# Kernel optimization log

Measured on AMD Instinct MI355X. Metric: run time of the kernel, lower is better.

Reference implementation:

```python
import jax, jax.numpy as jnp
import numpy as np

B, S, HID = 2, 1024, 2048
H, D, KV = 32, 64, 8          # query heads, head dim, kv heads (GQA)
INNER = H * D                 # 2048
KV_DIM = KV * D               # 512


def setup_inputs() -> dict:
    key = jax.random.key(0)
    ks = jax.random.split(key, 12)
    s = 0.02
    return {
        "query": jax.random.normal(ks[0], (B, S, HID), jnp.float32),
        "key": jax.random.normal(ks[1], (B, S, HID), jnp.float32),
        "value": jax.random.normal(ks[2], (B, S, HID), jnp.float32),
        "mask": jnp.zeros((B, 1, S, S), jnp.float32),
        "position_bias": jax.random.normal(ks[3], (1, H, S, S), jnp.float32),
        "Wq": jax.random.normal(ks[4], (HID, INNER), jnp.float32) * s,
        "bq": jnp.zeros((INNER,), jnp.float32),
        "Wk": jax.random.normal(ks[5], (HID, KV_DIM), jnp.float32) * s,
        "bk": jnp.zeros((KV_DIM,), jnp.float32),
        "Wv": jax.random.normal(ks[6], (HID, KV_DIM), jnp.float32) * s,
        "bv": jnp.zeros((KV_DIM,), jnp.float32),
        "Wo": jax.random.normal(ks[7], (INNER, HID), jnp.float32) * s,
        "bo": jnp.zeros((HID,), jnp.float32),
    }


def reference(query, key, value, mask, position_bias, Wq, bq, Wk, bk, Wv, bv, Wo, bo):
    # projections (torch nn.Linear equivalent, weights stored [in,out])
    q = (query @ Wq + bq).reshape(B, S, H, D)     # [B,S,H,D]
    k = (key @ Wk + bk).reshape(B, S, KV, D)      # [B,S,KV,D]
    v = (value @ Wv + bv).reshape(B, S, KV, D)
    rep = H // KV
    k = jnp.repeat(k, rep, axis=2)                # GQA repeat_kv -> [B,S,H,D]
    v = jnp.repeat(v, rep, axis=2)
    scores = jnp.einsum("bqhd,bkhd->bhqk", q, k)  # [B,H,S,S]
    scores = (scores + position_bias) * (1.0 / jnp.sqrt(jnp.float32(D)))
    scores = scores + mask
    probs = jax.nn.softmax(scores.astype(jnp.float32), axis=-1).astype(q.dtype)
    out = jnp.einsum("bhqk,bkhd->bqhd", probs, v).reshape(B, S, INNER)
    return out @ Wo + bo                          # [B,S,HID]
```

## Files before the change

kernel.cpp:

```cpp
#include <hip/hip_runtime.h>
#include <stdint.h>


#define DEVI __device__ __forceinline__

typedef __attribute__((ext_vector_type(8))) short bf16x8;
typedef __attribute__((ext_vector_type(4))) float f32x4;
typedef __attribute__((ext_vector_type(4))) float flt4;
typedef __attribute__((ext_vector_type(8))) unsigned short u16x8;
typedef __attribute__((ext_vector_type(4))) unsigned short u16x4;

DEVI unsigned short f2bf(float f){
  union{float f;uint32_t u;}v; v.f=f;
  uint32_t u=v.u;
  u += 0x7FFFu + ((u>>16)&1u);
  return (unsigned short)(u>>16);
}

DEVI uint32_t cvt_pk_bf16(float lo, float hi){
  uint32_t r;
  asm("v_cvt_pk_bf16_f32 %0, %1, %2" : "=v"(r) : "v"(lo), "v"(hi));
  return r;
}

DEVI float fexp2(float x){
#if __has_builtin(__builtin_amdgcn_exp2f)
  return __builtin_amdgcn_exp2f(x);
#else
  return exp2f(x);
#endif
}

DEVI void gload16(const void* g, void* l){
  __builtin_amdgcn_global_load_lds((const __attribute__((address_space(1))) void*)g,
                                   (__attribute__((address_space(3))) void*)l, 16, 0, 0);
}

__global__ void prep_k(const float* __restrict__ q, const float* __restrict__ k,
                       const float* __restrict__ v,
                       unsigned short* __restrict__ qb, unsigned short* __restrict__ kb,
                       unsigned short* __restrict__ vb,
                       const float* __restrict__ Wq, const float* __restrict__ Wk,
                       const float* __restrict__ Wv, const float* __restrict__ Wo,
                       unsigned short* __restrict__ WqT, unsigned short* __restrict__ WkT,
                       unsigned short* __restrict__ WvT, unsigned short* __restrict__ WoT){
  __shared__ float tile[64][65];
  int bid = blockIdx.x;
  if (bid < 6144){
    int z = bid>>11;
    int i = (bid&2047)*256 + threadIdx.x;
    const float* src = z==0 ? q : (z==1 ? k : v);
    unsigned short* dst = z==0 ? qb : (z==1 ? kb : vb);
    const flt4* s = (const flt4*)src;
    flt4 a = s[2*i], b = s[2*i+1];
    u16x8 o;
    o[0]=f2bf(a.x); o[1]=f2bf(a.y); o[2]=f2bf(a.z); o[3]=f2bf(a.w);
    o[4]=f2bf(b.x); o[5]=f2bf(b.y); o[6]=f2bf(b.z); o[7]=f2bf(b.w);
    ((u16x8*)dst)[i] = o;
    return;
  }
  int id = bid - 6144;
  const int K = 2048;
  const float* W; unsigned short* WT; int N, tt;
  if (id < 1024)      { W=Wq; WT=WqT; N=2048; tt=id; }
  else if (id < 1280) { W=Wk; WT=WkT; N=512;  tt=id-1024; }
  else if (id < 1536) { W=Wv; WT=WvT; N=512;  tt=id-1280; }
  else                { W=Wo; WT=WoT; N=2048; tt=id-1536; }
  int sh = (N==2048) ? 5 : 3;
  int n0 = (tt & ((1<<sh)-1))*64, k0 = (tt >> sh)*64;
  int t = threadIdx.x;
  int r = t>>4, c4 = (t&15)*4;
  #pragma unroll
  for (int i=0;i<4;i++){
    flt4 vv = *(const flt4*)&W[(size_t)(k0 + r + i*16)*N + n0 + c4];
    tile[r+i*16][c4+0]=vv.x; tile[r+i*16][c4+1]=vv.y; tile[r+i*16][c4+2]=vv.z; tile[r+i*16][c4+3]=vv.w;
  }
  __syncthreads();
  #pragma unroll
  for (int i=0;i<4;i++){
    int rn = r + i*16;
    u16x4 o;
    o[0]=f2bf(tile[c4+0][rn]); o[1]=f2bf(tile[c4+1][rn]);
    o[2]=f2bf(tile[c4+2][rn]); o[3]=f2bf(tile[c4+3][rn]);
    *(u16x4*)&WT[(size_t)(n0+rn)*K + k0 + c4] = o;
  }
}

#define GEMM64_KSTEP(A_, BT_, K_)                                              \
    __syncthreads();                                                           \
    _Pragma("unroll")                                                          \
    for (int j=0;j<2;j++){                                                     \
      int cid = (j*4+w)*64 + l;                                                \
      int row = cid>>3, sl = cid&7;                                            \
      int gsl = sl ^ (row&7);                                                  \
      gload16(&A_ [(size_t)(m0+row)*K_ + k0 + gsl*8], &As[(j*4+w)*512]);       \
      gload16(&BT_[(size_t)(n0+row)*K_ + k0 + gsl*8], &Bs[(j*4+w)*512]);       \
    }                                                                          \
    __syncthreads();                                                           \
    _Pragma("unroll")                                                          \
    for (int kk=0;kk<2;kk++){                                                  \
      bf16x8 af[2], bfv[2];                                                    \
      _Pragma("unroll")                                                        \
      for (int mt=0;mt<2;mt++){                                                \
        int row = wr+mt*16+lq;                                                 \
        af[mt] = *(const bf16x8*)&As[row*64 + (((kk*4+lg)^(lq&7))*8)];         \
      }                                                                        \
      _Pragma("unroll")                                                        \
      for (int nt=0;nt<2;nt++){                                                \
        int row = wc+nt*16+lq;                                                 \
        bfv[nt] = *(const bf16x8*)&Bs[row*64 + (((kk*4+lg)^(lq&7))*8)];        \
      }                                                                        \
      _Pragma("unroll")                                                        \
      for (int mt=0;mt<2;mt++)                                                 \
        _Pragma("unroll")                                                      \
        for (int nt=0;nt<2;nt++)                                               \
          acc[mt][nt] = __builtin_amdgcn_mfma_f32_16x16x32_bf16(af[mt], bfv[nt], acc[mt][nt], 0,0,0); \
    }

__global__ __launch_bounds__(256) void qkv64(const unsigned short* __restrict__ qbf,
    const unsigned short* __restrict__ kbf, const unsigned short* __restrict__ vbf,
    const unsigned short* __restrict__ WqT, const unsigned short* __restrict__ WkT,
    const unsigned short* __restrict__ WvT,
    const float* __restrict__ bq, const float* __restrict__ bk, const float* __restrict__ bv,
    unsigned short* __restrict__ Qp, unsigned short* __restrict__ Kp, unsigned short* __restrict__ VTb){
  __shared__ unsigned short As[64*64];
  __shared__ unsigned short Bs[64*64];
  const int K = 2048;
  int id = blockIdx.x;
  const unsigned short *A, *BT; const float* bias; int N, op, tt;
  if (id < 1024)      { op=0; A=qbf; BT=WqT; bias=bq; N=2048; tt=id; }
  else if (id < 1280) { op=1; A=kbf; BT=WkT; bias=bk; N=512;  tt=id-1024; }
  else                { op=2; A=vbf; BT=WvT; bias=bv; N=512;  tt=id-1280; }
  int sh = (N==2048) ? 5 : 3;
  int n0 = (tt & ((1<<sh)-1))*64, m0 = (tt >> sh)*64;
  int t = threadIdx.x, w = t>>6, l = t&63;
  int lq = l&15, lg = l>>4;
  int wr = (w>>1)*32, wc = (w&1)*32;
  f32x4 acc[2][2] = {};
  for (int k0=0;k0<K;k0+=64){
    GEMM64_KSTEP(A, BT, K)
  }
  #pragma unroll
  for (int nt=0;nt<2;nt++){
    int col = n0 + wc + nt*16 + lq;
    float bvl = bias[col];
    #pragma unroll
    for (int mt=0;mt<2;mt++){
      #pragma unroll
      for (int r=0;r<4;r++){
        int row = m0 + wr + mt*16 + lg*4 + r;
        float v = acc[mt][nt][r] + bvl;
        if (op==0)      Qp[(size_t)row*2048 + col] = f2bf(v);
        else if (op==1) Kp[(size_t)row*512 + col] = f2bf(v);
        else {
          int b = row>>10, s = row&1023;
          VTb[((size_t)(b*512 + col)<<10) + s] = f2bf(v);
        }
      }
    }
  }
}

__global__ __launch_bounds__(256) void oproj64(const unsigned short* __restrict__ A,
    const unsigned short* __restrict__ BT, const float* __restrict__ bias,
    float* __restrict__ Cout){
  __shared__ unsigned short As[64*64];
  __shared__ unsigned short Bs[64*64];
  const int K = 2048, N = 2048;
  int n0 = blockIdx.x*64, m0 = blockIdx.y*64;
  int t = threadIdx.x, w = t>>6, l = t&63;
  int lq = l&15, lg = l>>4;
  int wr = (w>>1)*32, wc = (w&1)*32;
  f32x4 acc[2][2] = {};
  for (int k0=0;k0<K;k0+=64){
    GEMM64_KSTEP(A, BT, K)
  }
  #pragma unroll
  for (int nt=0;nt<2;nt++){
    int col = n0 + wc + nt*16 + lq;
    float bvl = bias[col];
    #pragma unroll
    for (int mt=0;mt<2;mt++){
      #pragma unroll
      for (int r=0;r<4;r++){
        int row = m0 + wr + mt*16 + lg*4 + r;
        Cout[(size_t)row*N + col] = acc[mt][nt][r] + bvl;
      }
    }
  }
}

__global__ __launch_bounds__(512,4) void attn_k(const unsigned short* __restrict__ Q,
    const unsigned short* __restrict__ Kp, const unsigned short* __restrict__ VT,
    const float* __restrict__ pbias, const float* __restrict__ mask,
    unsigned short* __restrict__ Oout){
  __shared__ unsigned short Ks[2][4096];
  __shared__ unsigned short VTs[2][4096];
  __shared__ float Ms[2][2048];
  __shared__ unsigned short Pb[8][1024];
  int t=threadIdx.x, w=t>>6, l=t&63;
  int phys = blockIdx.x;
  int lin = (phys&7)*64 + (phys>>3);
  int qb = lin>>4, kv = (lin>>1)&7, b = lin&1;
  int h = kv*4 + (w&3);
  int qhalf = w>>2;
  int lq = l&15, lg = l>>4;
  int q0 = qb*32 + qhalf*16;
  int mr = qhalf*16 + lq;
  bf16x8 qf0, qf1;
  {
    const unsigned short* qp = &Q[((size_t)(b*1024 + q0 + lq))*2048 + h*64 + lg*8];
    qf0 = *(const bf16x8*)qp;
    qf1 = *(const bf16x8*)(qp + 32);
  }
  const float* pbase  = &pbias[((size_t)h*1024 + (q0+lq))*1024];
  const float* maskWG = &mask [((size_t)(b*1024 + qb*32))*1024];
  f32x4 oacc[4] = {};
  float psum = 0.f;
  const float L2E   = 1.4426950408889634f;
  const float SCL2E = 0.125f*1.4426950408889634f;
  const float NFM   = -16.0f*1.4426950408889634f;
  unsigned short* pw = &Pb[w][0];
  int swz = (lq&7)<<3;

  flt4 RA[4], RB[4], comb[4];

#define ATTN_STAGE(buf_, kt_)                                                           \
  {                                                                                     \
    int c = w*64 + l;                                                                   \
    int krow = c>>3, ksl = (c&7)^(krow&7);                                              \
    gload16(&Kp[((size_t)(b*1024 + (kt_)*64 + krow))*512 + kv*64 + ksl*8], &Ks[buf_][w*512]);          \
    gload16(&VT[((size_t)(b*512 + kv*64 + krow))*1024 + (size_t)((kt_)*64 + ksl*8)], &VTs[buf_][w*512]);\
    int mrow = c>>4, msl = (c&15)^(mrow&7);                                             \
    gload16(&maskWG[(size_t)mrow*1024 + (kt_)*64 + msl*4], &Ms[buf_][w*256]);           \
  }

#define ATTN_RAW(RP_, kt_)                                                              \
  _Pragma("unroll")                                                                     \
  for (int nt=0;nt<4;nt++)                                                              \
    RP_[nt] = *(const flt4*)&pbase[(kt_)*64 + nt*16 + lg*4];

#define ATTN_COMBINE(RP_, cur_)                                                         \
  _Pragma("unroll")                                                                     \
  for (int nt=0;nt<4;nt++){                                                             \
    flt4 m4 = *(const flt4*)&Ms[cur_][mr*64 + (((nt*4+lg)^(mr&7))<<2)];                 \
    _Pragma("unroll")                                                                   \
    for (int r=0;r<4;r++)                                                               \
      comb[nt][r] = fmaf(RP_[nt][r], SCL2E, fmaf(m4[r], L2E, NFM));                     \
  }

#define ATTN_COMPUTE(P_)                                                                \
  {                                                                                     \
    f32x4 sacc[4] = {};                                                                 \
    __builtin_amdgcn_s_setprio(1);                                                      \
    _Pragma("unroll")                                                                   \
    for (int nt=0;nt<4;nt++){                                                           \
      int row = nt*16 + lq;                                                             \
      bf16x8 kf0 = *(const bf16x8*)&Ks[P_][row*64 + (( lg    ^ (row&7))*8)];            \
      bf16x8 kf1 = *(const bf16x8*)&Ks[P_][row*64 + (((4+lg) ^ (row&7))*8)];            \
      sacc[nt] = __builtin_amdgcn_mfma_f32_16x16x32_bf16(kf0, qf0, sacc[nt], 0,0,0);    \
      sacc[nt] = __builtin_amdgcn_mfma_f32_16x16x32_bf16(kf1, qf1, sacc[nt], 0,0,0);    \
    }                                                                                   \
    __builtin_amdgcn_s_setprio(0);                                                      \
    _Pragma("unroll")                                                                   \
    for (int nt=0;nt<4;nt++){                                                           \
      float p0 = fexp2(fmaf(sacc[nt][0], SCL2E, comb[nt][0]));                          \
      float p1 = fexp2(fmaf(sacc[nt][1], SCL2E, comb[nt][1]));                          \
      float p2 = fexp2(fmaf(sacc[nt][2], SCL2E, comb[nt][2]));                          \
      float p3 = fexp2(fmaf(sacc[nt][3], SCL2E, comb[nt][3]));                          \
      psum += (p0+p1)+(p2+p3);                                                          \
      uint2 pk;                                                                         \
      pk.x = cvt_pk_bf16(p0,p1);                                                        \
      pk.y = cvt_pk_bf16(p2,p3);                                                        \
      *(uint2*)&pw[lq*64 + ((nt*16 + lg*4) ^ swz)] = pk;                                \
    }                                                                                   \
    _Pragma("unroll")                                                                   \
    for (int kk=0;kk<2;kk++){                                                           \
      bf16x8 pa = *(const bf16x8*)&pw[lq*64 + ((kk*32 + lg*8) ^ swz)];                  \
      __builtin_amdgcn_s_setprio(1);                                                    \
      _Pragma("unroll")                                                                 \
      for (int nt=0;nt<4;nt++){                                                         \
        int vrow = nt*16 + lq;                                                          \
        bf16x8 vf = *(const bf16x8*)&VTs[P_][vrow*64 + (((kk*4+lg) ^ (vrow&7))*8)];     \
        oacc[nt] = __builtin_amdgcn_mfma_f32_16x16x32_bf16(pa, vf, oacc[nt], 0,0,0);    \
      }                                                                                 \
      __builtin_amdgcn_s_setprio(0);                                                    \
    }                                                                                   \
  }

#define TILE(kt_, cur_, RP_, DOSTAGE, DORAW, VMFULL)                                    \
  {                                                                                     \
    if (DOSTAGE) ATTN_STAGE((cur_)^1, (kt_)+1)                                          \
    if (VMFULL) { asm volatile("s_waitcnt vmcnt(7)" ::: "memory"); }                    \
    else        { asm volatile("s_waitcnt vmcnt(0)" ::: "memory"); }                    \
    __builtin_amdgcn_s_barrier();                                                       \
    ATTN_COMBINE(RP_, cur_)                                                             \
    if (DORAW) ATTN_RAW(RP_, (kt_)+2)                                                   \
    ATTN_COMPUTE(cur_)                                                                  \
    __builtin_amdgcn_s_barrier();                                                       \
  }

  ATTN_STAGE(0, 0)
  ATTN_RAW(RA, 0)
  ATTN_RAW(RB, 1)

  for (int kb=0; kb<14; kb+=2){
    TILE(kb+0, 0, RA, 1, 1, 1)
    TILE(kb+1, 1, RB, 1, 1, 1)
  }
  TILE(14, 0, RA, 1, 0, 1)
  TILE(15, 1, RB, 0, 0, 0)

  float lsum = psum;
  lsum += __shfl_xor(lsum, 16);
  lsum += __shfl_xor(lsum, 32);
  #pragma unroll
  for (int r=0;r<4;r++){
    float lr = __shfl(lsum, lg*4 + r);
    float linv = 1.f/lr;
    int qrow = q0 + lg*4 + r;
    #pragma unroll
    for (int nt=0;nt<4;nt++){
      Oout[((size_t)(b*1024 + qrow))*2048 + h*64 + nt*16 + lq] = f2bf(oacc[nt][r]*linv);
    }
  }
#undef TILE
#undef ATTN_COMPUTE
#undef ATTN_COMBINE
#undef ATTN_RAW
#undef ATTN_STAGE
}

extern "C" void kernel_launch(void* const* d_in, const int* in_sizes, int n_in,
                              void* d_out, int out_size, void* d_ws, size_t ws_size,
                              hipStream_t stream){
  (void)in_sizes; (void)n_in; (void)out_size; (void)ws_size;
  const float* query = (const float*)d_in[0];
  const float* key   = (const float*)d_in[1];
  const float* value = (const float*)d_in[2];
  const float* mask  = (const float*)d_in[3];
  const float* pbias = (const float*)d_in[4];
  const float* Wq = (const float*)d_in[5];
  const float* bq = (const float*)d_in[6];
  const float* Wk = (const float*)d_in[7];
  const float* bk = (const float*)d_in[8];
  const float* Wv = (const float*)d_in[9];
  const float* bv = (const float*)d_in[10];
  const float* Wo = (const float*)d_in[11];
  const float* bo = (const float*)d_in[12];
  char* ws = (char*)d_ws;
  const size_t MB = (size_t)1<<20;
  unsigned short* qbf = (unsigned short*)(ws + 0*MB);
  unsigned short* kbf = (unsigned short*)(ws + 8*MB);
  unsigned short* vbf = (unsigned short*)(ws + 16*MB);
  unsigned short* WqT = (unsigned short*)(ws + 24*MB);
  unsigned short* WkT = (unsigned short*)(ws + 32*MB);
  unsigned short* WvT = (unsigned short*)(ws + 34*MB);
  unsigned short* WoT = (unsigned short*)(ws + 36*MB);
  unsigned short* Qp  = (unsigned short*)(ws + 44*MB);
  unsigned short* Kp  = (unsigned short*)(ws + 52*MB);
  unsigned short* VTb = (unsigned short*)(ws + 54*MB);
  unsigned short* Aout= (unsigned short*)(ws + 56*MB);

  prep_k<<<8704,256,0,stream>>>(query, key, value, qbf, kbf, vbf,
                                Wq, Wk, Wv, Wo, WqT, WkT, WvT, WoT);
  qkv64<<<1536,256,0,stream>>>(qbf, kbf, vbf, WqT, WkT, WvT, bq, bk, bv, Qp, Kp, VTb);
  attn_k<<<512,512,0,stream>>>(Qp, Kp, VTb, pbias, mask, Aout);
  oproj64<<<dim3(32,32),256,0,stream>>>(Aout, WoT, bo, (float*)d_out);
}
```

Before: 152.6 us.

## Process both batches per attention workgroup to reuse position-bias loads

Each attention workgroup now handles both batch elements for the same (q-block, kv-head), so every position_bias tile is loaded from global memory once and used twice. Key tiles shrink from 64 to 32 columns so K, V and mask for both batches fit the shared buffers, and the loop grows to 32 tiles. The grid halves to 256 blocks and the occupancy hint drops to 2, which lowers parallelism and may leave compute units underused. In exchange, reads of the largest input (the fp32 bias) are halved.

```diff
diff --git a/kernel.cpp b/kernel.cpp
--- a/kernel.cpp
+++ b/kernel.cpp
@@ -190,142 +190,161 @@
   }
 }
 
-__global__ __launch_bounds__(512,4) void attn_k(const unsigned short* __restrict__ Q,
+__global__ __launch_bounds__(512,2) void attn_k(const unsigned short* __restrict__ Q,
     const unsigned short* __restrict__ Kp, const unsigned short* __restrict__ VT,
     const float* __restrict__ pbias, const float* __restrict__ mask,
     unsigned short* __restrict__ Oout){
-  __shared__ unsigned short Ks[2][4096];
+  __shared__ unsigned short Ks[2][2][2048];
   __shared__ unsigned short VTs[2][4096];
-  __shared__ float Ms[2][2048];
-  __shared__ unsigned short Pb[8][1024];
+  __shared__ float Ms[2][2][1024];
+  __shared__ unsigned short Pb[8][512];
   int t=threadIdx.x, w=t>>6, l=t&63;
-  int phys = blockIdx.x;
-  int lin = (phys&7)*64 + (phys>>3);
-  int qb = lin>>4, kv = (lin>>1)&7, b = lin&1;
+  int kv = blockIdx.x & 7;
+  int qb = blockIdx.x >> 3;
   int h = kv*4 + (w&3);
   int qhalf = w>>2;
   int lq = l&15, lg = l>>4;
   int q0 = qb*32 + qhalf*16;
   int mr = qhalf*16 + lq;
-  bf16x8 qf0, qf1;
+  bf16x8 qfA0, qfA1, qfB0, qfB1;
   {
-    const unsigned short* qp = &Q[((size_t)(b*1024 + q0 + lq))*2048 + h*64 + lg*8];
-    qf0 = *(const bf16x8*)qp;
-    qf1 = *(const bf16x8*)(qp + 32);
-  }
-  const float* pbase  = &pbias[((size_t)h*1024 + (q0+lq))*1024];
-  const float* maskWG = &mask [((size_t)(b*1024 + qb*32))*1024];
-  f32x4 oacc[4] = {};
-  float psum = 0.f;
+    const unsigned short* qp = &Q[((size_t)(q0 + lq))*2048 + h*64 + lg*8];
+    qfA0 = *(const bf16x8*)qp;  qfA1 = *(const bf16x8*)(qp + 32);
+    qp += (size_t)1024*2048;
+    qfB0 = *(const bf16x8*)qp;  qfB1 = *(const bf16x8*)(qp + 32);
+  }
+  const float* pbase = &pbias[((size_t)h*1024 + (q0+lq))*1024];
+  f32x4 oaccA[4] = {}, oaccB[4] = {};
+  float psumA = 0.f, psumB = 0.f;
   const float L2E   = 1.4426950408889634f;
   const float SCL2E = 0.125f*1.4426950408889634f;
   const float NFM   = -16.0f*1.4426950408889634f;
   unsigned short* pw = &Pb[w][0];
-  int swz = (lq&7)<<3;
-
-  flt4 RA[4], RB[4], comb[4];
-
-#define ATTN_STAGE(buf_, kt_)                                                           \
-  {                                                                                     \
-    int c = w*64 + l;                                                                   \
-    int krow = c>>3, ksl = (c&7)^(krow&7);                                              \
-    gload16(&Kp[((size_t)(b*1024 + (kt_)*64 + krow))*512 + kv*64 + ksl*8], &Ks[buf_][w*512]);          \
-    gload16(&VT[((size_t)(b*512 + kv*64 + krow))*1024 + (size_t)((kt_)*64 + ksl*8)], &VTs[buf_][w*512]);\
-    int mrow = c>>4, msl = (c&15)^(mrow&7);                                             \
-    gload16(&maskWG[(size_t)mrow*1024 + (kt_)*64 + msl*4], &Ms[buf_][w*256]);           \
-  }
-
-#define ATTN_RAW(RP_, kt_)                                                              \
-  _Pragma("unroll")                                                                     \
-  for (int nt=0;nt<4;nt++)                                                              \
-    RP_[nt] = *(const flt4*)&pbase[(kt_)*64 + nt*16 + lg*4];
-
-#define ATTN_COMBINE(RP_, cur_)                                                         \
-  _Pragma("unroll")                                                                     \
-  for (int nt=0;nt<4;nt++){                                                             \
-    flt4 m4 = *(const flt4*)&Ms[cur_][mr*64 + (((nt*4+lg)^(mr&7))<<2)];                 \
-    _Pragma("unroll")                                                                   \
-    for (int r=0;r<4;r++)                                                               \
-      comb[nt][r] = fmaf(RP_[nt][r], SCL2E, fmaf(m4[r], L2E, NFM));                     \
-  }
-
-#define ATTN_COMPUTE(P_)                                                                \
-  {                                                                                     \
-    f32x4 sacc[4] = {};                                                                 \
-    __builtin_amdgcn_s_setprio(1);                                                      \
-    _Pragma("unroll")                                                                   \
-    for (int nt=0;nt<4;nt++){                                                           \
-      int row = nt*16 + lq;                                                             \
-      bf16x8 kf0 = *(const bf16x8*)&Ks[P_][row*64 + (( lg    ^ (row&7))*8)];            \
-      bf16x8 kf1 = *(const bf16x8*)&Ks[P_][row*64 + (((4+lg) ^ (row&7))*8)];            \
-      sacc[nt] = __builtin_amdgcn_mfma_f32_16x16x32_bf16(kf0, qf0, sacc[nt], 0,0,0);    \
-      sacc[nt] = __builtin_amdgcn_mfma_f32_16x16x32_bf16(kf1, qf1, sacc[nt], 0,0,0);    \
-    }                                                                                   \
-    __builtin_amdgcn_s_setprio(0);                                                      \
-    _Pragma("unroll")                                                                   \
-    for (int nt=0;nt<4;nt++){                                                           \
-      float p0 = fexp2(fmaf(sacc[nt][0], SCL2E, comb[nt][0]));                          \
-      float p1 = fexp2(fmaf(sacc[nt][1], SCL2E, comb[nt][1]));                          \
-      float p2 = fexp2(fmaf(sacc[nt][2], SCL2E, comb[nt][2]));                          \
-      float p3 = fexp2(fmaf(sacc[nt][3], SCL2E, comb[nt][3]));                          \
-      psum += (p0+p1)+(p2+p3);                                                          \
-      uint2 pk;                                                                         \
-      pk.x = cvt_pk_bf16(p0,p1);                                                        \
-      pk.y = cvt_pk_bf16(p2,p3);                                                        \
-      *(uint2*)&pw[lq*64 + ((nt*16 + lg*4) ^ swz)] = pk;                                \
-    }                                                                                   \
-    _Pragma("unroll")                                                                   \
-    for (int kk=0;kk<2;kk++){                                                           \
-      bf16x8 pa = *(const bf16x8*)&pw[lq*64 + ((kk*32 + lg*8) ^ swz)];                  \
-      __builtin_amdgcn_s_setprio(1);                                                    \
-      _Pragma("unroll")                                                                 \
-      for (int nt=0;nt<4;nt++){                                                         \
-        int vrow = nt*16 + lq;                                                          \
-        bf16x8 vf = *(const bf16x8*)&VTs[P_][vrow*64 + (((kk*4+lg) ^ (vrow&7))*8)];     \
-        oacc[nt] = __builtin_amdgcn_mfma_f32_16x16x32_bf16(pa, vf, oacc[nt], 0,0,0);    \
-      }                                                                                 \
-      __builtin_amdgcn_s_setprio(0);                                                    \
-    }                                                                                   \
-  }
-
-#define TILE(kt_, cur_, RP_, DOSTAGE, DORAW, VMFULL)                                    \
-  {                                                                                     \
-    if (DOSTAGE) ATTN_STAGE((cur_)^1, (kt_)+1)                                          \
-    if (VMFULL) { asm volatile("s_waitcnt vmcnt(7)" ::: "memory"); }                    \
-    else        { asm volatile("s_waitcnt vmcnt(0)" ::: "memory"); }                    \
-    __builtin_amdgcn_s_barrier();                                                       \
-    ATTN_COMBINE(RP_, cur_)                                                             \
-    if (DORAW) ATTN_RAW(RP_, (kt_)+2)                                                   \
-    ATTN_COMPUTE(cur_)                                                                  \
-    __builtin_amdgcn_s_barrier();                                                       \
+  int swz = (lq&3)<<3;
+
+  flt4 RA[2], RB[2], comb[2][2];
+
+#define ATTN_STAGE(buf_, kt_)                                                            \
+  {                                                                                      \
+    { int bb = w>>2; int row = (w&3)*8 + (l>>3); int ch = (l&7)^(row&7);                 \
+      gload16(&Kp[((size_t)(bb*1024 + (kt_)*32 + row))*512 + kv*64 + ch*8],              \
+              &Ks[buf_][0][0] + w*512); }                                                \
+    { int row = w*8 + (l>>3); int g = (l&7)^(row&7);                                     \
+      gload16(&VT[((size_t)((g>>2)*512 + kv*64 + row))*1024 + (kt_)*32 + (g&3)*8],       \
+              &VTs[buf_][0] + w*512); }                                                  \
+    { int bb = w>>2; int row = (w&3)*8 + (l>>3); int ch = (l&7)^(row&7);                 \
+      gload16(&mask[((size_t)(bb*1024 + qb*32 + row))*1024 + (kt_)*32 + ch*4],           \
+              &Ms[buf_][0][0] + w*256); }                                                \
+  }
+
+#define ATTN_RAW(RP_, kt_)                                                               \
+  _Pragma("unroll")                                                                      \
+  for (int nt=0;nt<2;nt++)                                                               \
+    RP_[nt] = *(const flt4*)&pbase[(kt_)*32 + nt*16 + lg*4];
+
+#define ATTN_COMBINE(RP_, cur_)                                                          \
+  _Pragma("unroll")                                                                      \
+  for (int bb=0;bb<2;bb++)                                                               \
+    _Pragma("unroll")                                                                    \
+    for (int nt=0;nt<2;nt++){                                                            \
+      flt4 m4 = *(const flt4*)&Ms[cur_][bb][mr*32 + (((nt*4+lg)^(mr&7))<<2)];            \
+      _Pragma("unroll")                                                                  \
+      for (int r=0;r<4;r++)                                                              \
+        comb[bb][nt][r] = fmaf(RP_[nt][r], SCL2E, fmaf(m4[r], L2E, NFM));                \
+    }
+
+#define COMPUTE_BATCH(P_, bb_, QF0_, QF1_, OACC_, PS_)                                   \
+  {                                                                                      \
+    f32x4 sacc[2] = {};                                                                  \
+    __builtin_amdgcn_s_setprio(1);                                                       \
+    _Pragma("unroll")                                                                    \
+    for (int nt=0;nt<2;nt++){                                                            \
+      int row = nt*16 + lq;                                                              \
+      bf16x8 kf0 = *(const bf16x8*)&Ks[P_][bb_][row*64 + (( lg    ^ (row&7))*8)];        \
+      bf16x8 kf1 = *(const bf16x8*)&Ks[P_][bb_][row*64 + (((4+lg) ^ (row&7))*8)];        \
+      sacc[nt] = __builtin_amdgcn_mfma_f32_16x16x32_bf16(kf0, QF0_, sacc[nt], 0,0,0);    \
+      sacc[nt] = __builtin_amdgcn_mfma_f32_16x16x32_bf16(kf1, QF1_, sacc[nt], 0,0,0);    \
+    }                                                                                    \
+    __builtin_amdgcn_s_setprio(0);                                                       \
+    _Pragma("unroll")                                                                    \
+    for (int nt=0;nt<2;nt++){                                                            \
+      float p0 = fexp2(fmaf(sacc[nt][0], SCL2E, comb[bb_][nt][0]));                      \
+      float p1 = fexp2(fmaf(sacc[nt][1], SCL2E, comb[bb_][nt][1]));                      \
+      float p2 = fexp2(fmaf(sacc[nt][2], SCL2E, comb[bb_][nt][2]));                      \
+      float p3 = fexp2(fmaf(sacc[nt][3], SCL2E, comb[bb_][nt][3]));                      \
+      PS_ += (p0+p1)+(p2+p3);                                                            \
+      uint2 pk;                                                                          \
+      pk.x = cvt_pk_bf16(p0,p1);                                                         \
+      pk.y = cvt_pk_bf16(p2,p3);                                                         \
+      *(uint2*)&pw[lq*32 + ((nt*16 + lg*4) ^ swz)] = pk;                                 \
+    }                                                                                    \
+    {                                                                                    \
+      bf16x8 pa = *(const bf16x8*)&pw[lq*32 + ((lg*8) ^ swz)];                           \
+      __builtin_amdgcn_s_setprio(1);                                                     \
+      _Pragma("unroll")                                                                  \
+      for (int nt=0;nt<4;nt++){                                                          \
+        int vrow = nt*16 + lq;                                                           \
+        bf16x8 vf = *(const bf16x8*)&VTs[P_][vrow*64 + ((((bb_)*4+lg) ^ (vrow&7))*8)];   \
+        OACC_[nt] = __builtin_amdgcn_mfma_f32_16x16x32_bf16(pa, vf, OACC_[nt], 0,0,0);   \
+      }                                                                                  \
+      __builtin_amdgcn_s_setprio(0);                                                     \
+    }                                                                                    \
+  }
+
+#define TILE(kt_, cur_, RP_, DOSTAGE, DORAW, VMFULL)                                     \
+  {                                                                                      \
+    if (DOSTAGE) ATTN_STAGE((cur_)^1, (kt_)+1)                                           \
+    if (VMFULL) { asm volatile("s_waitcnt vmcnt(5)" ::: "memory"); }                     \
+    else        { asm volatile("s_waitcnt vmcnt(0)" ::: "memory"); }                     \
+    __builtin_amdgcn_s_barrier();                                                        \
+    ATTN_COMBINE(RP_, cur_)                                                              \
+    if (DORAW) ATTN_RAW(RP_, (kt_)+2)                                                    \
+    COMPUTE_BATCH(cur_, 0, qfA0, qfA1, oaccA, psumA)                                     \
+    COMPUTE_BATCH(cur_, 1, qfB0, qfB1, oaccB, psumB)                                     \
+    __builtin_amdgcn_s_barrier();                                                        \
   }
 
   ATTN_STAGE(0, 0)
   ATTN_RAW(RA, 0)
   ATTN_RAW(RB, 1)
 
-  for (int kb=0; kb<14; kb+=2){
+  for (int kb=0; kb<30; kb+=2){
     TILE(kb+0, 0, RA, 1, 1, 1)
     TILE(kb+1, 1, RB, 1, 1, 1)
   }
-  TILE(14, 0, RA, 1, 0, 1)
-  TILE(15, 1, RB, 0, 0, 0)
-
-  float lsum = psum;
-  lsum += __shfl_xor(lsum, 16);
-  lsum += __shfl_xor(lsum, 32);
-  #pragma unroll
-  for (int r=0;r<4;r++){
-    float lr = __shfl(lsum, lg*4 + r);
-    float linv = 1.f/lr;
-    int qrow = q0 + lg*4 + r;
+  TILE(30, 0, RA, 1, 0, 1)
+  TILE(31, 1, RB, 0, 0, 0)
+
+  {
+    float lsum = psumA;
+    lsum += __shfl_xor(lsum, 16);
+    lsum += __shfl_xor(lsum, 32);
     #pragma unroll
-    for (int nt=0;nt<4;nt++){
-      Oout[((size_t)(b*1024 + qrow))*2048 + h*64 + nt*16 + lq] = f2bf(oacc[nt][r]*linv);
+    for (int r=0;r<4;r++){
+      float lr = __shfl(lsum, lg*4 + r);
+      float linv = 1.f/lr;
+      int qrow = q0 + lg*4 + r;
+      #pragma unroll
+      for (int nt=0;nt<4;nt++)
+        Oout[((size_t)qrow)*2048 + h*64 + nt*16 + lq] = f2bf(oaccA[nt][r]*linv);
+    }
+  }
+  {
+    float lsum = psumB;
+    lsum += __shfl_xor(lsum, 16);
+    lsum += __shfl_xor(lsum, 32);
+    #pragma unroll
+    for (int r=0;r<4;r++){
+      float lr = __shfl(lsum, lg*4 + r);
+      float linv = 1.f/lr;
+      int qrow = q0 + lg*4 + r;
+      #pragma unroll
+      for (int nt=0;nt<4;nt++)
+        Oout[((size_t)(1024 + qrow))*2048 + h*64 + nt*16 + lq] = f2bf(oaccB[nt][r]*linv);
     }
   }
 #undef TILE
-#undef ATTN_COMPUTE
+#undef COMPUTE_BATCH
 #undef ATTN_COMBINE
 #undef ATTN_RAW
 #undef ATTN_STAGE
@@ -365,6 +384,6 @@
   prep_k<<<8704,256,0,stream>>>(query, key, value, qbf, kbf, vbf,
                                 Wq, Wk, Wv, Wo, WqT, WkT, WvT, WoT);
   qkv64<<<1536,256,0,stream>>>(qbf, kbf, vbf, WqT, WkT, WvT, bq, bk, bv, Qp, Kp, VTb);
-  attn_k<<<512,512,0,stream>>>(Qp, Kp, VTb, pbias, mask, Aout);
+  attn_k<<<256,512,0,stream>>>(Qp, Kp, VTb, pbias, mask, Aout);
   oproj64<<<dim3(32,32),256,0,stream>>>(Aout, WoT, bo, (float*)d_out);
 }
```

Measured after the change: 151.0 us. About the same (-1.1%).
